# Kernel optimization log

Measured on AMD Instinct MI355X. Metric: run time of the kernel, lower is better.

The kernel has to match this reference:

```python
import jax, jax.numpy as jnp
import numpy as np

HEADS = 8
GS = 16
C = 512
E = 512
SCALE = (E / HEADS) ** -0.5
PNAMES = ['sa_qkv_w','sa_qkv_b','sa_pa_w','sa_pa_b','sa_ln1_g','sa_ln1_b','sa_f1_w','sa_f1_b','sa_f2_w','sa_f2_b','sa_ln2_g','sa_ln2_b','sa_c1_w','sa_c1_b','sa_c2_w','sa_c2_b','sa_bn_g','sa_bn_b','ca_q_w','ca_q_b','ca_k_w','ca_k_b','ca_v_w','ca_v_b','ca_pa_w','ca_pa_b','p_q_w','p_q_b','p_k_w','p_k_b','p_v_w','p_v_b','p_pa_w','p_pa_b','p_ln_g','p_ln_b','p_lin_w','p_lin_b']


def _ln(x, g, b, eps=1e-5):
    m = x.mean(-1, keepdims=True)
    v = jnp.var(x, axis=-1, keepdims=True)
    return (x - m) / jnp.sqrt(v + eps) * g + b


def _conv1x1(x, w, b):
    return jnp.einsum('bchw,oc->bohw', x, w) + b[None, :, None, None]


def _up_ac(x, out=GS):
    # bilinear upsample, align_corners=True (nn.UpsamplingBilinear2d)
    H = x.shape[2]
    pos = jnp.arange(out) * (H - 1) / (out - 1)
    lo = jnp.floor(pos).astype(jnp.int32)
    hi = jnp.minimum(lo + 1, H - 1)
    w = (pos - lo).astype(x.dtype)
    xr = x[:, :, lo, :] * (1 - w)[None, None, :, None] + x[:, :, hi, :] * w[None, None, :, None]
    return xr[:, :, :, lo] * (1 - w) + xr[:, :, :, hi] * w


def _asri(x, p):
    # Sequence_ASRI: GAP tokens -> attention over the batch axis -> pixel-shuffle back
    B = x.shape[0]; ch = E // HEADS
    gap = x.mean((2, 3))                                             # [B,C]
    qkv = (gap @ p['sa_qkv_w'].T + p['sa_qkv_b']).reshape(B, 4, ch, HEADS).transpose(1, 3, 0, 2)  # [4,H,B,ch]
    q, k, v, skip = qkv[0], qkv[1], qkv[2], qkv[3]
    attn = jax.nn.softmax(jnp.einsum('hbc,hdc->hbd', q, k) * SCALE, -1)  # [H,B,B]
    o = jnp.einsum('hbd,hdc->hbc', attn, v)
    merge = lambda t: t.transpose(1, 2, 0).reshape(B, E)             # 'head b c -> b (c head)'
    a = merge(o) @ p['sa_pa_w'].T + p['sa_pa_b'] + merge(skip)
    h = jax.nn.relu(_ln(a, p['sa_ln1_g'], p['sa_ln1_b']) @ p['sa_f1_w'].T + p['sa_f1_b'])
    a = h @ p['sa_f2_w'].T + p['sa_f2_b'] + a
    s = _ln(a, p['sa_ln2_g'], p['sa_ln2_b']) @ p['sa_c1_w'].T + p['sa_c1_b']  # [B,C*16]
    s = _up_ac(s.reshape(B, C, 4, 4))                                 # pixel shuffle p1=p2=4 then bilinear to 16x16
    s = _conv1x1(s, p['sa_c2_w'], p['sa_c2_b'])
    # BatchNorm2d in eval mode (running_mean=0, running_var=1, eps=1e-5)
    s = s / np.float32(np.sqrt(1.0 + 1e-5)) * p['sa_bn_g'][None, :, None, None] + p['sa_bn_b'][None, :, None, None]
    return x + jax.nn.relu(s)


def _sscm(x1, x2, p):
    # Sequence_SSCM: GAP-token q/k over batch axis, full spatial v
    B = x1.shape[0]; ch = E // HEADS
    q = (x1.mean((2, 3)) @ p['ca_q_w'].T + p['ca_q_b']).reshape(B, ch, HEADS).transpose(2, 0, 1)  # [H,B,ch]
    k = (x2.mean((2, 3)) @ p['ca_k_w'].T + p['ca_k_b']).reshape(B, ch, HEADS).transpose(2, 0, 1)
    v = _conv1x1(x2, p['ca_v_w'], p['ca_v_b']).reshape(B, ch, HEADS, GS, GS).transpose(2, 0, 1, 3, 4).reshape(HEADS, B, ch * GS * GS)
    attn = jax.nn.softmax(jnp.einsum('hbc,hdc->hbd', q, k) * SCALE, -1)  # [H,B,B]
    o = jnp.einsum('hbd,hdm->hbm', attn, v)
    o = o.reshape(HEADS, B, ch, GS, GS).transpose(1, 2, 0, 3, 4).reshape(B, E, GS, GS)
    return jax.nn.relu(_conv1x1(o, p['ca_pa_w'], p['ca_pa_b']))


def _pixel(x1, x2, p):
    # Pixel_SSCM: pixel-wise cross-batch attention (no scale -- matches source)
    B = x1.shape[0]; ch = E // HEADS; N = GS * GS
    split = lambda t: t.reshape(B, ch, HEADS, N).transpose(2, 0, 3, 1)   # 'b (c head) h w -> head b (h w) c'
    q = split(_conv1x1(x1, p['p_q_w'], p['p_q_b']))                      # [H,B,N,ch]
    k = split(_conv1x1(x2, p['p_k_w'], p['p_k_b']))
    v = split(_conv1x1(x2, p['p_v_w'], p['p_v_b'])).reshape(HEADS, B * N, ch)
    attn = jax.nn.softmax(jnp.einsum('hbnc,hqmc->hbqnm', q, k), -1)      # [H,B,B,N,N]
    attn = attn.transpose(1, 0, 3, 2, 4).reshape(B, HEADS, N, B * N)     # 'head b q h w -> b head h (q w)'
    o = jnp.einsum('bhnm,hmc->bhnc', attn, v)
    o = o.transpose(0, 3, 1, 2).reshape(B, E, GS, GS)                    # 'b head (h w) c -> b (c head) h w'
    o = _conv1x1(o, p['p_pa_w'], p['p_pa_b']) + x1
    t = o.reshape(B, C, N).transpose(0, 2, 1)                            # [B,N,C]
    t = jax.nn.relu(_ln(t, p['p_ln_g'], p['p_ln_b']) @ p['p_lin_w'].T + p['p_lin_b'])
    return t.transpose(0, 2, 1).reshape(B, C, GS, GS)


def _hrlm(p, xs, xq):
    sa_s = _asri(xs, p)
    sa_q = _asri(xq, p)
    ca_s = _sscm(sa_s, sa_q, p)
    ca_q = _sscm(sa_q, sa_s, p)
    return _pixel(sa_s, ca_q, p), _pixel(sa_q, ca_s, p)


def setup_inputs():
    key = jax.random.key(0)
    ks = iter(jax.random.split(key, 64))
    w = lambda *s: (jax.random.normal(next(ks), s) * 0.02).astype(jnp.float32)
    z = lambda n: jnp.zeros((n,), jnp.float32)
    o = lambda n: jnp.ones((n,), jnp.float32)
    return dict(
        fea_support=jax.random.normal(next(ks), (8, C, GS, GS), jnp.float32),
        fea_query=jax.random.normal(next(ks), (8, C, GS, GS), jnp.float32),
        sa_qkv_w=w(4 * E, C), sa_qkv_b=z(4 * E),
        sa_pa_w=w(E, E), sa_pa_b=z(E),
        sa_ln1_g=o(E), sa_ln1_b=z(E),
        sa_f1_w=w(E, E), sa_f1_b=z(E), sa_f2_w=w(E, E), sa_f2_b=z(E),
        sa_ln2_g=o(E), sa_ln2_b=z(E),
        sa_c1_w=w(C * 16, E), sa_c1_b=z(C * 16),
        sa_c2_w=w(C, E), sa_c2_b=z(C),
        sa_bn_g=o(C), sa_bn_b=z(C),
        ca_q_w=w(E, C), ca_q_b=z(E), ca_k_w=w(E, C), ca_k_b=z(E),
        ca_v_w=w(E, C), ca_v_b=z(E), ca_pa_w=w(C, E), ca_pa_b=z(C),
        p_q_w=w(E, C), p_q_b=z(E), p_k_w=w(E, C), p_k_b=z(E),
        p_v_w=w(E, C), p_v_b=z(E), p_pa_w=w(C, E), p_pa_b=z(C),
        p_ln_g=o(C), p_ln_b=z(C), p_lin_w=w(C, C), p_lin_b=z(C),
    )


def reference(fea_support, fea_query, sa_qkv_w, sa_qkv_b, sa_pa_w, sa_pa_b, sa_ln1_g, sa_ln1_b, sa_f1_w, sa_f1_b, sa_f2_w, sa_f2_b, sa_ln2_g, sa_ln2_b, sa_c1_w, sa_c1_b, sa_c2_w, sa_c2_b, sa_bn_g, sa_bn_b, ca_q_w, ca_q_b, ca_k_w, ca_k_b, ca_v_w, ca_v_b, ca_pa_w, ca_pa_b, p_q_w, p_q_b, p_k_w, p_k_b, p_v_w, p_v_b, p_pa_w, p_pa_b, p_ln_g, p_ln_b, p_lin_w, p_lin_b):
    p = dict(zip(PNAMES, (sa_qkv_w, sa_qkv_b, sa_pa_w, sa_pa_b, sa_ln1_g, sa_ln1_b, sa_f1_w, sa_f1_b, sa_f2_w, sa_f2_b, sa_ln2_g, sa_ln2_b, sa_c1_w, sa_c1_b, sa_c2_w, sa_c2_b, sa_bn_g, sa_bn_b, ca_q_w, ca_q_b, ca_k_w, ca_k_b, ca_v_w, ca_v_b, ca_pa_w, ca_pa_b, p_q_w, p_q_b, p_k_w, p_k_b, p_v_w, p_v_b, p_pa_w, p_pa_b, p_ln_g, p_ln_b, p_lin_w, p_lin_b)))
    return _hrlm(p, fea_support, fea_query)
```

## Files before the change

kernel.cpp:

```cpp
#include <hip/hip_runtime.h>
#include <cmath>

#define IMG 131072
#define BIGF 1048576

#define CF_RELU 1
#define CF_RES  2
#define CF_BN   4

typedef __attribute__((ext_vector_type(8))) short short8;
typedef __attribute__((ext_vector_type(4))) short short4v;
typedef __attribute__((ext_vector_type(4))) float f32x4;

__device__ __forceinline__ float wave_sum(float v){
    #pragma unroll
    for (int off = 32; off; off >>= 1) v += __shfl_xor(v, off);
    return v;
}

__device__ __forceinline__ unsigned short bf16_rn(float x){
    union { float f; unsigned u; } v; v.f = x;
    unsigned r = v.u + 0x7FFF + ((v.u >> 16) & 1);
    return (unsigned short)(r >> 16);
}
__device__ __forceinline__ float bf16_to_f(unsigned short h){
    union { float f; unsigned u; } v; v.u = ((unsigned)h) << 16;
    return v.f;
}

struct GapJobs  { const float* x[2]; float* o[2]; };
struct G8Job    { const float* in; const float* W; const float* bias; const float* add; float* out; };
struct G8Jobs   { G8Job j[4]; };
struct AAJobs   { const float* qkv[2]; float* om[2]; };
struct LnJobs   { const float* in[2]; float* out[2]; };
struct UpJobs   { const float* in[2]; float* out[2]; };
struct SAJobs   { const float* q8[2]; const float* k8[2]; float* aw[2]; };
struct SPJobs   { const float* aw[2]; const float* v[2]; float* out[2]; };
struct ZJobs    { float* p[2]; };
struct ConvJob  { const float* X; const float* W; const float* B; const float* R;
                  const float* bng; const float* bnb; float* O; int flags; };
struct ConvJobs { ConvJob j[6]; };
struct PixJob   { const float* Q; const float* K; const float* V; float* O; };
struct PixJobs  { PixJob j[2]; };

__global__ __launch_bounds__(64) void k_gap(GapJobs jo){
    const int br = blockIdx.y;
    const int bc = blockIdx.x;
    const int lane = threadIdx.x;
    const float* p = jo.x[br] + (size_t)bc * 256;
    float s = p[lane] + p[lane + 64] + p[lane + 128] + p[lane + 192];
    s = wave_sum(s);
    if (lane == 0) jo.o[br][bc] = s * (1.0f / 256.0f);
}

__global__ __launch_bounds__(64) void k_gemm8(G8Jobs jo, int add_off, int add_stride, int O, int relu){
    const G8Job j = jo.j[blockIdx.y];
    const int o = blockIdx.x;
    const int lane = threadIdx.x;
    const float* wr = j.W + (size_t)o * 512;
    float acc[8] = {0,0,0,0,0,0,0,0};
    #pragma unroll
    for (int i = 0; i < 8; i++){
        float w = wr[lane + 64*i];
        #pragma unroll
// ... 61 lines not shown
    }
}

__global__ __launch_bounds__(256) void k_up(UpJobs jo){
    const int br = blockIdx.y;
    const int idx = blockIdx.x*256 + threadIdx.x;
    const int x = idx & 15, y = (idx >> 4) & 15, bc = idx >> 8;
    float px = (float)(x*3) / 15.0f, py = (float)(y*3) / 15.0f;
    int lx = (int)px, ly = (int)py;
    float wx = px - lx, wy = py - ly;
    int hx = min(lx+1, 3), hy = min(ly+1, 3);
    const float* p = jo.in[br] + (size_t)bc * 16;
    float v00 = p[ly*4+lx], v01 = p[ly*4+hx], v10 = p[hy*4+lx], v11 = p[hy*4+hx];
    float a0 = v00*(1.f-wy) + v10*wy;
    float a1 = v01*(1.f-wy) + v11*wy;
    jo.out[br][idx] = a0*(1.f-wx) + a1*wx;
}

__global__ __launch_bounds__(256) void k_zero(ZJobs jo){
    jo.p[blockIdx.y][(size_t)blockIdx.x*256 + threadIdx.x] = 0.f;
}

#define LDK 40
__device__ __forceinline__ void convm_body(
    const float* __restrict__ Xb, const float* __restrict__ W,
    const float* __restrict__ bias, const float* __restrict__ resb,
    const float* __restrict__ bng, const float* __restrict__ bnb, float bninv,
    float* __restrict__ outb, int flags, int o0, int n0, unsigned short* lds)
{
    const int tid512 = threadIdx.x;
    const int g   = tid512 >> 8;
    const int tid = tid512 & 255;
    unsigned short* sAh = lds + g*10240;
    unsigned short* sAl = sAh + 2560;
    unsigned short* sBh = sAl + 2560;
    unsigned short* sBl = sBh + 2560;
    const int wv = tid >> 6, lane = tid & 63;
    const int quad = lane >> 4, l16 = lane & 15;
    const int wo = (wv >> 1) * 32, wn = (wv & 1) * 32;
    const int so  = tid >> 2, sk8 = (tid & 3) * 8;
    const int sp  = tid & 15, sn  = (tid >> 4) * 4;

    const float* wrow = W + (size_t)(o0 + so)*512 + g*256 + sk8;
    const float* xrow = Xb + (size_t)(g*256 + 2*sp)*256 + n0 + sn;

    f32x4 acc[2][2] = {};
    float4 a0 = *(const float4*)(wrow);
    float4 a1 = *(const float4*)(wrow + 4);
    float4 x0 = *(const float4*)(xrow);
    float4 x1 = *(const float4*)(xrow + 256);

    for (int k0 = 0; k0 < 256; k0 += 32){
        __syncthreads();
        {
            float wa[8] = {a0.x,a0.y,a0.z,a0.w,a1.x,a1.y,a1.z,a1.w};
            #pragma unroll
            for (int j = 0; j < 4; j++){
                unsigned short h0 = bf16_rn(wa[2*j]);
                unsigned short h1 = bf16_rn(wa[2*j+1]);
                unsigned short g0 = bf16_rn(wa[2*j]   - bf16_to_f(h0));
                unsigned short g1 = bf16_rn(wa[2*j+1] - bf16_to_f(h1));
                *(unsigned*)&sAh[so*LDK + sk8 + 2*j] = (unsigned)h0 | ((unsigned)h1 << 16);
                *(unsigned*)&sAl[so*LDK + sk8 + 2*j] = (unsigned)g0 | ((unsigned)g1 << 16);
            }
            float xe[4] = {x0.x,x0.y,x0.z,x0.w};
            float xo[4] = {x1.x,x1.y,x1.z,x1.w};
            #pragma unroll
            for (int j = 0; j < 4; j++){
                unsigned short h0 = bf16_rn(xe[j]);
                unsigned short h1 = bf16_rn(xo[j]);
                unsigned short g0 = bf16_rn(xe[j] - bf16_to_f(h0));
                unsigned short g1 = bf16_rn(xo[j] - bf16_to_f(h1));
                *(unsigned*)&sBh[(sn+j)*LDK + 2*sp] = (unsigned)h0 | ((unsigned)h1 << 16);
                *(unsigned*)&sBl[(sn+j)*LDK + 2*sp] = (unsigned)g0 | ((unsigned)g1 << 16);
            }
        }
        __syncthreads();
        if (k0 + 32 < 256){
            a0 = *(const float4*)(wrow + k0 + 32);
            a1 = *(const float4*)(wrow + k0 + 36);
            x0 = *(const float4*)(xrow + (size_t)(k0+32)*256);
            x1 = *(const float4*)(xrow + (size_t)(k0+32)*256 + 256);
        }
        short8 ah[2], al[2], bh[2], bl[2];
        #pragma unroll
        for (int t = 0; t < 2; t++){
            int ai = (wo + 16*t + l16)*LDK + quad*8;
            ah[t] = *(const short8*)&sAh[ai];
            al[t] = *(const short8*)&sAl[ai];
            int bi = (wn + 16*t + l16)*LDK + quad*8;
            bh[t] = *(const short8*)&sBh[bi];
            bl[t] = *(const short8*)&sBl[bi];
        }
        #pragma unroll
        for (int mt = 0; mt < 2; mt++){
            #pragma unroll
            for (int nt = 0; nt < 2; nt++){
// ... 7 lines not shown
    float* red = (float*)lds;
    if (g == 1){
        float* r = red + tid*20;
        #pragma unroll
        for (int mt = 0; mt < 2; mt++)
            #pragma unroll
            for (int nt = 0; nt < 2; nt++)
                *(f32x4*)(r + (mt*2+nt)*4) = acc[mt][nt];
    }
    __syncthreads();
    if (g == 0){
        float* r = red + tid*20;
        #pragma unroll
        for (int mt = 0; mt < 2; mt++)
            #pragma unroll
            for (int nt = 0; nt < 2; nt++){
                f32x4 o4 = *(const f32x4*)(r + (mt*2+nt)*4);
                acc[mt][nt] += o4;
            }
        #pragma unroll
        for (int mt = 0; mt < 2; mt++){
            #pragma unroll
            for (int nt = 0; nt < 2; nt++){
                const int n  = n0 + wn + 16*nt + l16;
                const int ob = o0 + wo + 16*mt + quad*4;
                #pragma unroll
                for (int rr = 0; rr < 4; rr++){
                    const int o = ob + rr;
                    float v = acc[mt][nt][rr] + bias[o];
                    if (flags & CF_BN)   v = v*(bninv*bng[o]) + bnb[o];
                    if (flags & CF_RELU) v = fmaxf(v, 0.f);
                    if (flags & CF_RES)  v += resb[(size_t)o*256 + n];
                    outb[(size_t)o*256 + n] = v;
                }
            }
        }
    }
}

__global__ __launch_bounds__(512) void k_convm(ConvJobs jo, float bninv)
{
    __shared__ unsigned short lds[20480];
    const int z = blockIdx.z;
    const ConvJob j = jo.j[z >> 3];
    const int b = z & 7;
    convm_body(j.X + (size_t)b*IMG, j.W, j.B, j.R ? j.R + (size_t)b*IMG : nullptr,
               j.bng, j.bnb, bninv, j.O + (size_t)b*IMG, j.flags,
               blockIdx.y*64, blockIdx.x*64, lds);
}

__global__ __launch_bounds__(64) void k_sscm_attn(SAJobs jo)
{
    const int br = blockIdx.y;
    const int h = blockIdx.x >> 3, b = blockIdx.x & 7, c = threadIdx.x;
    const int ci = c*8 + h;
    float qc = jo.q8[br][b*512 + ci];
    float s[8];
    #pragma unroll
    for (int d = 0; d < 8; d++){
        float p = qc * jo.k8[br][d*512 + ci];
        p = wave_sum(p);
        s[d] = p * 0.125f;
    }
// ... 7 lines not shown
    if (c < 8){
        float v = s[0];
        #pragma unroll
        for (int d = 1; d < 8; d++) if (c == d) v = s[d];
        jo.aw[br][blockIdx.x*8 + c] = v*r;
    }
}

__global__ __launch_bounds__(256) void k_sscm_apply(SPJobs jo)
{
    const int br = blockIdx.y;
    const int idx = blockIdx.x*256 + threadIdx.x;
    const int pix = idx & 255, e = (idx >> 8) & 511, b = idx >> 17;
    const int h = e & 7;
    const float* aw = jo.aw[br] + (h*8 + b)*8;
    const float* v = jo.v[br];
    float acc = 0.f;
    #pragma unroll
    for (int d = 0; d < 8; d++) acc += aw[d] * v[(size_t)d*IMG + (size_t)e*256 + pix];
    jo.out[br][idx] = acc;
}

__global__ __launch_bounds__(256) void k_pixel_mfma(PixJobs jo)
{
    __shared__ char smem[61440];
    unsigned short* sQh = (unsigned short*)smem;
    unsigned short* sQl = sQh + 2*64*40;
    unsigned short* sKh = sQl + 2*64*40;
    unsigned short* sKl = sKh + 2*128*40;
    unsigned short* sP  = (unsigned short*)smem;
    unsigned short* sVh = sP  + 4*64*40;
    unsigned short* sVl = sVh + 4*64*40;

    const int br = blockIdx.y >> 3, b = blockIdx.y & 7;
    const PixJob J = jo.j[br];
    const int nt = blockIdx.x & 3, d = blockIdx.x >> 2;
    const int h = blockIdx.z;
    const int tid = threadIdx.x;
    const int wv = tid >> 6, lane = tid & 63;
    const int quad = lane >> 4, l16 = lane & 15;
    const int n0 = nt * 64;
    const size_t bQ = (size_t)b * IMG;
    const size_t bK = (size_t)d * IMG;

    {
        const int q = tid & 63, c0 = tid >> 6;
        #pragma unroll
        for (int r = 0; r < 16; r++){
            int c = c0 + 4*r;
            float v = J.Q[bQ + (size_t)(c*8+h)*256 + n0 + q];
            unsigned short hi = bf16_rn(v);
            unsigned short lo = bf16_rn(v - bf16_to_f(hi));
            int idx = (c>>5)*2560 + q*40 + (c&31);
            sQh[idx] = hi; sQl[idx] = lo;
        }
    }
    {
        const int mloc = tid & 127, cb0 = tid >> 7;
        #pragma unroll
        for (int p = 0; p < 4; p++){
            int cb = cb0 + 2*p;
            short8 hi8, lo8;
            #pragma unroll
            for (int j = 0; j < 8; j++){
                float v = J.K[bK + (size_t)((cb*8+j)*8+h)*256 + mloc];
                unsigned short hv = bf16_rn(v);
                hi8[j] = (short)hv;
                lo8[j] = (short)bf16_rn(v - bf16_to_f(hv));
            }
            int idx = (cb>>2)*5120 + mloc*40 + (cb&3)*8;
            *(short8*)&sKh[idx] = hi8;
            *(short8*)&sKl[idx] = lo8;
        }
    }
    __syncthreads();

    short8 bqh[2], bql[2];
    #pragma unroll
    for (int ks = 0; ks < 2; ks++){
        int idx = ks*2560 + (wv*16 + l16)*40 + quad*8;
        bqh[ks] = *(const short8*)&sQh[idx];
        bql[ks] = *(const short8*)&sQl[idx];
    }

    f32x4 S[16] = {};
    #pragma unroll
    for (int hm = 0; hm < 2; hm++){
        if (hm == 1){
            __syncthreads();
            const int mloc = tid & 127, cb0 = tid >> 7;
            #pragma unroll
            for (int p = 0; p < 4; p++){
                int cb = cb0 + 2*p;
                short8 hi8, lo8;
                #pragma unroll
                for (int j = 0; j < 8; j++){
                    float v = J.K[bK + (size_t)((cb*8+j)*8+h)*256 + 128 + mloc];
                    unsigned short hv = bf16_rn(v);
                    hi8[j] = (short)hv;
                    lo8[j] = (short)bf16_rn(v - bf16_to_f(hv));
                }
                int idx = (cb>>2)*5120 + mloc*40 + (cb&3)*8;
                *(short8*)&sKh[idx] = hi8;
                *(short8*)&sKl[idx] = lo8;
            }
            __syncthreads();
        }
        #pragma unroll
        for (int mtl = 0; mtl < 8; mtl++){
            #pragma unroll
            for (int ks = 0; ks < 2; ks++){
                int idx = ks*5120 + (mtl*16 + l16)*40 + quad*8;
                short8 ah = *(const short8*)&sKh[idx];
                short8 al = *(const short8*)&sKl[idx];
                S[hm*8+mtl] = __builtin_amdgcn_mfma_f32_16x16x32_bf16(ah, bqh[ks], S[hm*8+mtl], 0, 0, 0);
// ... 30 lines not shown
    #pragma unroll
    for (int hm = 0; hm < 2; hm++){
        #pragma unroll
        for (int mtl = 0; mtl < 8; mtl++){
            short4v p4;
            #pragma unroll
            for (int r = 0; r < 4; r++) p4[r] = (short)bf16_rn(S[hm*8+mtl][r]);
            int idx = (mtl>>1)*2560 + (wv*16 + l16)*40 + 16*(mtl&1) + quad*4;
            *(short4v*)&sP[idx] = p4;
        }
        {
            const int mp = tid & 63, c0 = tid >> 6;
            #pragma unroll
            for (int p = 0; p < 16; p++){
                int c = c0 + 4*p;
                float2 vv = *(const float2*)&J.V[bK + (size_t)(c*8+h)*256 + hm*128 + 2*mp];
                unsigned short h0 = bf16_rn(vv.x), h1 = bf16_rn(vv.y);
                unsigned short g0 = bf16_rn(vv.x - bf16_to_f(h0));
                unsigned short g1 = bf16_rn(vv.y - bf16_to_f(h1));
                int idx = (mp>>4)*2560 + c*40 + ((2*mp)&31);
                *(unsigned*)&sVh[idx] = (unsigned)h0 | ((unsigned)h1 << 16);
                *(unsigned*)&sVl[idx] = (unsigned)g0 | ((unsigned)g1 << 16);
            }
        }
        __syncthreads();
        #pragma unroll
        for (int ks = 0; ks < 4; ks++){
            int pidx = ks*2560 + (wv*16 + l16)*40 + quad*8;
            short8 bp = *(const short8*)&sP[pidx];
            #pragma unroll
            for (int ct = 0; ct < 4; ct++){
                int vidx = ks*2560 + (ct*16 + l16)*40 + quad*8;
                short8 vh = *(const short8*)&sVh[vidx];
                short8 vl = *(const short8*)&sVl[vidx];
                oac[ct] = __builtin_amdgcn_mfma_f32_16x16x32_bf16(vh, bp, oac[ct], 0, 0, 0);
                oac[ct] = __builtin_amdgcn_mfma_f32_16x16x32_bf16(vl, bp, oac[ct], 0, 0, 0);
            }
        }
        __syncthreads();
    }

    const int q = n0 + wv*16 + l16;
    #pragma unroll
    for (int ct = 0; ct < 4; ct++){
        #pragma unroll
        for (int r = 0; r < 4; r++){
            int c = ct*16 + quad*4 + r;
            unsafeAtomicAdd(&J.O[bQ + (size_t)(c*8+h)*256 + q], oac[ct][r]);
        }
    }
}

__global__ __launch_bounds__(64) void k_ln_pix(LnJobs jo,
    const float* __restrict__ g, const float* __restrict__ be)
{
    const int br = blockIdx.y;
    const int bn = blockIdx.x;
    const int b = bn >> 8, n = bn & 255;
    const int lane = threadIdx.x;
    const float* p = jo.in[br] + (size_t)b*IMG + n;
    float v[8]; float s = 0.f;
    #pragma unroll
    for (int i = 0; i < 8; i++){ v[i] = p[(size_t)(lane + 64*i)*256]; s += v[i]; }
    s = wave_sum(s);
    float mean = s * (1.f/512.f);
    float q = 0.f;
    #pragma unroll
    for (int i = 0; i < 8; i++){ float d = v[i]-mean; q += d*d; }
    q = wave_sum(q);
    float rstd = rsqrtf(q*(1.f/512.f) + 1e-5f);
    #pragma unroll
    for (int i = 0; i < 8; i++){
        int c = lane + 64*i;
        jo.out[br][(size_t)b*IMG + (size_t)c*256 + n] = (v[i]-mean)*rstd*g[c] + be[c];
    }
}

extern "C" void kernel_launch(void* const* d_in, const int* in_sizes, int n_in,
                              void* d_out, int out_size, void* d_ws, size_t ws_size,
                              hipStream_t stream)
{
    const float* xs    = (const float*)d_in[0];
    const float* xq    = (const float*)d_in[1];
    const float* qkvw  = (const float*)d_in[2];  const float* qkvb = (const float*)d_in[3];
    const float* paw   = (const float*)d_in[4];  const float* pab  = (const float*)d_in[5];
    const float* ln1g  = (const float*)d_in[6];  const float* ln1b = (const float*)d_in[7];
    const float* f1w   = (const float*)d_in[8];  const float* f1b  = (const float*)d_in[9];
    const float* f2w   = (const float*)d_in[10]; const float* f2b  = (const float*)d_in[11];
    const float* ln2g  = (const float*)d_in[12]; const float* ln2b = (const float*)d_in[13];
    const float* c1w   = (const float*)d_in[14]; const float* c1b  = (const float*)d_in[15];
    const float* c2w   = (const float*)d_in[16]; const float* c2b  = (const float*)d_in[17];
    const float* bng   = (const float*)d_in[18]; const float* bnb  = (const float*)d_in[19];
    const float* caqw  = (const float*)d_in[20]; const float* caqb = (const float*)d_in[21];
    const float* cakw  = (const float*)d_in[22]; const float* cakb = (const float*)d_in[23];
    const float* cavw  = (const float*)d_in[24]; const float* cavb = (const float*)d_in[25];
    const float* capw  = (const float*)d_in[26]; const float* capb = (const float*)d_in[27];
    const float* pqw   = (const float*)d_in[28]; const float* pqb  = (const float*)d_in[29];
    const float* pkw   = (const float*)d_in[30]; const float* pkb  = (const float*)d_in[31];
    const float* pvw   = (const float*)d_in[32]; const float* pvb  = (const float*)d_in[33];
    const float* ppw   = (const float*)d_in[34]; const float* ppb  = (const float*)d_in[35];
    const float* plng  = (const float*)d_in[36]; const float* plnb = (const float*)d_in[37];
    const float* plinw = (const float*)d_in[38]; const float* plinb= (const float*)d_in[39];

    const size_t SMF = 262144;
    float* ws = (float*)d_ws;
    float* smb = ws;
    float* B[12];
    for (int i = 0; i < 12; i++) B[i] = ws + SMF + (size_t)i*BIGF;
    float* sa_s = B[0]; float* sa_q = B[1];
    float* ca_s = B[2]; float* ca_q = B[3];
    const bool paired_pixel = ws_size >= (SMF + 12*(size_t)BIGF)*sizeof(float) + 1024;

    auto SM = [&](int br){ return smb + (size_t)br*131072; };
    auto GAP=[&](int br){ return SM(br); };            auto QKV=[&](int br){ return SM(br)+4096; };
    auto OM =[&](int br){ return SM(br)+20480; };      auto AA =[&](int br){ return SM(br)+24576; };
    auto HB =[&](int br){ return SM(br)+28672; };      auto A2 =[&](int br){ return SM(br)+32768; };
    auto LNB=[&](int br){ return SM(br)+36864; };      auto S8 =[&](int br){ return SM(br)+40960; };
    auto ATW=[&](int br){ return SM(br)+106496; };     auto Q8 =[&](int br){ return SM(br)+107008; };
    auto K8 =[&](int br){ return SM(br)+111104; };

    const float bninv = 1.0f / sqrtf(1.0f + 1e-5f);
    float* out0 = (float*)d_out;
    float* out1 = out0 + (size_t)BIGF;

    {
        GapJobs gj = {{xs, xq}, {GAP(0), GAP(1)}};
        k_gap<<<dim3(4096,2), 64, 0, stream>>>(gj);
        G8Jobs qj = {{{GAP(0), qkvw, qkvb, nullptr, QKV(0)}, {GAP(1), qkvw, qkvb, nullptr, QKV(1)}}};
        k_gemm8<<<dim3(2048,2), 64, 0, stream>>>(qj, 0, 0, 2048, 0);
        AAJobs aj = {{QKV(0), QKV(1)}, {OM(0), OM(1)}};
        k_asri_attn<<<dim3(64,2), 64, 0, stream>>>(aj);
        G8Jobs pj = {{{OM(0), paw, pab, QKV(0), AA(0)}, {OM(1), paw, pab, QKV(1), AA(1)}}};
        k_gemm8<<<dim3(512,2), 64, 0, stream>>>(pj, 1536, 2048, 512, 0);
        LnJobs l1 = {{AA(0), AA(1)}, {LNB(0), LNB(1)}};
        k_ln8<<<dim3(8,2), 64, 0, stream>>>(l1, ln1g, ln1b);
        G8Jobs fj = {{{LNB(0), f1w, f1b, nullptr, HB(0)}, {LNB(1), f1w, f1b, nullptr, HB(1)}}};
        k_gemm8<<<dim3(512,2), 64, 0, stream>>>(fj, 0, 0, 512, 1);
        G8Jobs f2j = {{{HB(0), f2w, f2b, AA(0), A2(0)}, {HB(1), f2w, f2b, AA(1), A2(1)}}};
        k_gemm8<<<dim3(512,2), 64, 0, stream>>>(f2j, 0, 512, 512, 0);
        LnJobs l2 = {{A2(0), A2(1)}, {LNB(0), LNB(1)}};
        k_ln8<<<dim3(8,2), 64, 0, stream>>>(l2, ln2g, ln2b);
        G8Jobs cj = {{{LNB(0), c1w, c1b, nullptr, S8(0)}, {LNB(1), c1w, c1b, nullptr, S8(1)}}};
        k_gemm8<<<dim3(8192,2), 64, 0, stream>>>(cj, 0, 0, 8192, 0);
        UpJobs uj = {{S8(0), S8(1)}, {B[4], B[5]}};
        k_up<<<dim3(4096,2), 256, 0, stream>>>(uj);
        ConvJobs c2j = {};
        c2j.j[0] = {B[4], c2w, c2b, xs, bng, bnb, sa_s, CF_BN|CF_RELU|CF_RES};
        c2j.j[1] = {B[5], c2w, c2b, xq, bng, bnb, sa_q, CF_BN|CF_RELU|CF_RES};
        k_convm<<<dim3(4,8,16), 512, 0, stream>>>(c2j, bninv);
    }

    {
        GapJobs gj = {{sa_s, sa_q}, {GAP(0), GAP(1)}};
        k_gap<<<dim3(4096,2), 64, 0, stream>>>(gj);
        G8Jobs qj = {{{GAP(0), caqw, caqb, nullptr, Q8(0)},
                      {GAP(1), cakw, cakb, nullptr, K8(0)},
                      {GAP(1), caqw, caqb, nullptr, Q8(1)},
                      {GAP(0), cakw, cakb, nullptr, K8(1)}}};
        k_gemm8<<<dim3(512,4), 64, 0, stream>>>(qj, 0, 0, 512, 0);
        SAJobs sj = {{Q8(0), Q8(1)}, {K8(0), K8(1)}, {ATW(0), ATW(1)}};
        k_sscm_attn<<<dim3(64,2), 64, 0, stream>>>(sj);
        ConvJobs vj = {};
        vj.j[0] = {sa_q, cavw, cavb, nullptr, nullptr, nullptr, B[4], 0};
        vj.j[1] = {sa_s, cavw, cavb, nullptr, nullptr, nullptr, B[5], 0};
        k_convm<<<dim3(4,8,16), 512, 0, stream>>>(vj, 1.f);
        SPJobs pj = {{ATW(0), ATW(1)}, {B[4], B[5]}, {B[6], B[7]}};
        k_sscm_apply<<<dim3(4096,2), 256, 0, stream>>>(pj);
        ConvJobs aj = {};
        aj.j[0] = {B[6], capw, capb, nullptr, nullptr, nullptr, ca_s, CF_RELU};
        aj.j[1] = {B[7], capw, capb, nullptr, nullptr, nullptr, ca_q, CF_RELU};
        k_convm<<<dim3(4,8,16), 512, 0, stream>>>(aj, 1.f);
    }

    if (paired_pixel){
        ConvJobs qkvj = {};
        qkvj.j[0] = {sa_s, pqw, pqb, nullptr, nullptr, nullptr, B[4],  0};
        qkvj.j[1] = {ca_q, pkw, pkb, nullptr, nullptr, nullptr, B[5],  0};
        qkvj.j[2] = {ca_q, pvw, pvb, nullptr, nullptr, nullptr, B[6],  0};
        qkvj.j[3] = {sa_q, pqw, pqb, nullptr, nullptr, nullptr, B[8],  0};
        qkvj.j[4] = {ca_s, pkw, pkb, nullptr, nullptr, nullptr, B[9],  0};
        qkvj.j[5] = {ca_s, pvw, pvb, nullptr, nullptr, nullptr, B[10], 0};
        k_convm<<<dim3(4,8,48), 512, 0, stream>>>(qkvj, 1.f);
        ZJobs zj = {{B[7], B[11]}};
        k_zero<<<dim3(4096,2), 256, 0, stream>>>(zj);
        PixJobs pxj = {{{B[4], B[5], B[6], B[7]}, {B[8], B[9], B[10], B[11]}}};
        k_pixel_mfma<<<dim3(32,16,8), 256, 0, stream>>>(pxj);
        ConvJobs ppj = {};
        ppj.j[0] = {B[7],  ppw, ppb, sa_s, nullptr, nullptr, out0, CF_RES};
        ppj.j[1] = {B[11], ppw, ppb, sa_q, nullptr, nullptr, out1, CF_RES};
        k_convm<<<dim3(4,8,16), 512, 0, stream>>>(ppj, 1.f);
        LnJobs lj = {{out0, out1}, {B[4], B[8]}};
        k_ln_pix<<<dim3(2048,2), 64, 0, stream>>>(lj, plng, plnb);
        ConvJobs lnj = {};
        lnj.j[0] = {B[4], plinw, plinb, nullptr, nullptr, nullptr, out0, CF_RELU};
        lnj.j[1] = {B[8], plinw, plinb, nullptr, nullptr, nullptr, out1, CF_RELU};
        k_convm<<<dim3(4,8,16), 512, 0, stream>>>(lnj, 1.f);
    } else {
        auto pixel1 = [&](const float* x1, const float* x2, float* out){
            ConvJobs qkvj = {};
            qkvj.j[0] = {x1, pqw, pqb, nullptr, nullptr, nullptr, B[4], 0};
            qkvj.j[1] = {x2, pkw, pkb, nullptr, nullptr, nullptr, B[5], 0};
            qkvj.j[2] = {x2, pvw, pvb, nullptr, nullptr, nullptr, B[6], 0};
            k_convm<<<dim3(4,8,24), 512, 0, stream>>>(qkvj, 1.f);
            ZJobs zj = {{B[7], B[7]}};
            k_zero<<<dim3(4096,1), 256, 0, stream>>>(zj);
            PixJobs pxj = {{{B[4], B[5], B[6], B[7]}, {B[4], B[5], B[6], B[7]}}};
            k_pixel_mfma<<<dim3(32,8,8), 256, 0, stream>>>(pxj);
            ConvJobs ppj = {};
            ppj.j[0] = {B[7], ppw, ppb, x1, nullptr, nullptr, out, CF_RES};
            k_convm<<<dim3(4,8,8), 512, 0, stream>>>(ppj, 1.f);
            LnJobs lj = {{out, out}, {B[4], B[4]}};
            k_ln_pix<<<dim3(2048,1), 64, 0, stream>>>(lj, plng, plnb);
            ConvJobs lnj = {};
            lnj.j[0] = {B[4], plinw, plinb, nullptr, nullptr, nullptr, out, CF_RELU};
            k_convm<<<dim3(4,8,8), 512, 0, stream>>>(lnj, 1.f);
        };
        pixel1(sa_s, ca_q, out0);
        pixel1(sa_q, ca_s, out1);
    }

    (void)in_sizes; (void)n_in; (void)out_size;
}
```

Baseline: 480.7 us.

## Pre-split weights and activations into bf16 hi/lo pairs in producer epilogues

Weights are split once into bf16 hi/lo planes by a new kernel. Each producer kernel (upsample, conv epilogue, sscm_apply, layernorm, pixel attention output) now writes hi/lo bf16 planes directly, so the 1x1-conv GEMM and the pixel attention just copy pre-split data into LDS instead of converting fp32 in their inner loops. Intermediates move into a fixed global device pool, and the single-buffer fallback path is dropped. The cost is an extra split pass over the attention output and doubled writes for the split tensors. The weight split runs on every call.

```diff
diff --git a/kernel.cpp b/kernel.cpp
--- a/kernel.cpp
+++ b/kernel.cpp
@@ -3,13 +3,40 @@
 
 #define IMG 131072
 #define BIGF 1048576
-
-#define CF_RELU 1
-#define CF_RES  2
-#define CF_BN   4
+#define SBIG 1048576
+#define MB (1u<<20)
+#define TS (4u*MB)
+
+#define OFF_W   0u
+#define OFF_UP  (8u*MB)
+#define OFF_SAS (16u*MB)
+#define OFF_AP  (24u*MB)
+#define OFF_CA  (32u*MB)
+#define OFF_PQ  (40u*MB)
+#define OFF_PK  (48u*MB)
+#define OFF_PV  (56u*MB)
+#define OFF_OS  (64u*MB)
+#define OFF_LN  (72u*MB)
+#define OFF_FSA (80u*MB)
+#define OFF_FV  (88u*MB)
+#define OFF_FO  (96u*MB)
+
+__device__ __attribute__((aligned(256))) unsigned char g_pool[104u*MB];
+
+__device__ __forceinline__ unsigned short* SPL(size_t off){ return (unsigned short*)(g_pool + off); }
+__device__ __forceinline__ float* F32(size_t off){ return (float*)(g_pool + off); }
+
+#define CF_RELU  1
+#define CF_BN    2
+#define CF_RESE  4
+#define CF_RESP  8
+#define CF_OF32E 16
+#define CF_OF32P 32
+#define CF_OSPL  64
 
 typedef __attribute__((ext_vector_type(8))) short short8;
 typedef __attribute__((ext_vector_type(4))) short short4v;
+typedef __attribute__((ext_vector_type(4))) unsigned short ushort4v;
 typedef __attribute__((ext_vector_type(4))) float f32x4;
 
 __device__ __forceinline__ float wave_sum(float v){
@@ -17,7 +44,6 @@
     for (int off = 32; off; off >>= 1) v += __shfl_xor(v, off);
     return v;
 }
-
 __device__ __forceinline__ unsigned short bf16_rn(float x){
     union { float f; unsigned u; } v; v.f = x;
     unsigned r = v.u + 0x7FFF + ((v.u >> 16) & 1);
@@ -28,26 +54,66 @@
     return v.f;
 }
 
-struct GapJobs  { const float* x[2]; float* o[2]; };
+struct GapJobs  { const float* x[2]; size_t off[2]; float* o[2]; };
 struct G8Job    { const float* in; const float* W; const float* bias; const float* add; float* out; };
 struct G8Jobs   { G8Job j[4]; };
 struct AAJobs   { const float* qkv[2]; float* om[2]; };
 struct LnJobs   { const float* in[2]; float* out[2]; };
-struct UpJobs   { const float* in[2]; float* out[2]; };
+struct UpJobs   { const float* in[2]; };
 struct SAJobs   { const float* q8[2]; const float* k8[2]; float* aw[2]; };
-struct SPJobs   { const float* aw[2]; const float* v[2]; float* out[2]; };
-struct ZJobs    { float* p[2]; };
-struct ConvJob  { const float* X; const float* W; const float* B; const float* R;
-                  const float* bng; const float* bnb; float* O; int flags; };
+struct SPJobs   { const float* aw[2]; };
+struct W8       { const float* w[8]; };
+struct ConvJob  { size_t xoff, ooff, osoff, roff; const float* Rext; float* OextW;
+                  const float* Bp; int widx, flags; };
 struct ConvJobs { ConvJob j[6]; };
-struct PixJob   { const float* Q; const float* K; const float* V; float* O; };
-struct PixJobs  { PixJob j[2]; };
+struct PixLnJobs{ const float* in[2]; };
+
+__global__ __launch_bounds__(256) void k_splitw(W8 ws){
+    const int m = blockIdx.y;
+    const int i = (blockIdx.x*256 + threadIdx.x)*4;
+    float4 v = *(const float4*)(ws.w[m] + i);
+    unsigned short* WH = (unsigned short*)(g_pool + (size_t)m*1048576u);
+    unsigned short* WL = WH + 262144;
+    float vv[4] = {v.x, v.y, v.z, v.w};
+    ushort4v hi, lo;
+    #pragma unroll
+    for (int j = 0; j < 4; j++){
+        hi[j] = bf16_rn(vv[j]);
+        lo[j] = bf16_rn(vv[j] - bf16_to_f(hi[j]));
+    }
+    *(ushort4v*)&WH[i] = hi;
+    *(ushort4v*)&WL[i] = lo;
+}
+
+__global__ __launch_bounds__(256) void k_split_o(){
+    const int br = blockIdx.y;
+    const int i = (blockIdx.x*256 + threadIdx.x)*4;
+    const float* src = F32(OFF_FO + (size_t)br*TS);
+    unsigned short* H = SPL(OFF_OS + (size_t)br*TS);
+    float4 v = *(const float4*)(src + i);
+    float vv[4] = {v.x, v.y, v.z, v.w};
+    ushort4v hi, lo;
+    #pragma unroll
+    for (int j = 0; j < 4; j++){
+        hi[j] = bf16_rn(vv[j]);
+        lo[j] = bf16_rn(vv[j] - bf16_to_f(hi[j]));
+    }
+    *(ushort4v*)&H[i] = hi;
+    *(ushort4v*)&H[SBIG + i] = lo;
+}
+
+__global__ __launch_bounds__(256) void k_zero(){
+    float* p = F32(OFF_FO + (size_t)blockIdx.y*TS);
+    const int i = (blockIdx.x*256 + threadIdx.x)*4;
+    *(float4*)&p[i] = make_float4(0.f,0.f,0.f,0.f);
+}
 
 __global__ __launch_bounds__(64) void k_gap(GapJobs jo){
     const int br = blockIdx.y;
     const int bc = blockIdx.x;
     const int lane = threadIdx.x;
-    const float* p = jo.x[br] + (size_t)bc * 256;
+    const float* base = jo.x[br] ? jo.x[br] : F32(jo.off[br]);
+    const float* p = base + (size_t)bc * 256;
     float s = p[lane] + p[lane + 64] + p[lane + 128] + p[lane + 192];
     s = wave_sum(s);
     if (lane == 0) jo.o[br][bc] = s * (1.0f / 256.0f);
@@ -139,20 +205,23 @@
     float v00 = p[ly*4+lx], v01 = p[ly*4+hx], v10 = p[hy*4+lx], v11 = p[hy*4+hx];
     float a0 = v00*(1.f-wy) + v10*wy;
     float a1 = v01*(1.f-wy) + v11*wy;
-    jo.out[br][idx] = a0*(1.f-wx) + a1*wx;
-}
-
-__global__ __launch_bounds__(256) void k_zero(ZJobs jo){
-    jo.p[blockIdx.y][(size_t)blockIdx.x*256 + threadIdx.x] = 0.f;
+    float val = a0*(1.f-wx) + a1*wx;
+    unsigned short* H = SPL(OFF_UP + (size_t)br*TS);
+    unsigned short hi = bf16_rn(val);
+    H[idx] = hi;
+    H[SBIG + idx] = bf16_rn(val - bf16_to_f(hi));
 }
 
 #define LDK 40
-__device__ __forceinline__ void convm_body(
-    const float* __restrict__ Xb, const float* __restrict__ W,
-    const float* __restrict__ bias, const float* __restrict__ resb,
-    const float* __restrict__ bng, const float* __restrict__ bnb, float bninv,
-    float* __restrict__ outb, int flags, int o0, int n0, unsigned short* lds)
+__global__ __launch_bounds__(512) void k_convm(ConvJobs jo,
+    const float* __restrict__ bng, const float* __restrict__ bnb, float bninv)
 {
+    __shared__ unsigned short lds[20480];
+    const int z = blockIdx.z;
+    const ConvJob j = jo.j[z >> 3];
+    const int b = z & 7;
+    const int o0 = blockIdx.y*64, n0 = blockIdx.x*64;
+
     const int tid512 = threadIdx.x;
     const int g   = tid512 >> 8;
     const int tid = tid512 & 255;
@@ -166,46 +235,40 @@
     const int so  = tid >> 2, sk8 = (tid & 3) * 8;
     const int sp  = tid & 15, sn  = (tid >> 4) * 4;
 
-    const float* wrow = W + (size_t)(o0 + so)*512 + g*256 + sk8;
-    const float* xrow = Xb + (size_t)(g*256 + 2*sp)*256 + n0 + sn;
+    const unsigned short* WB = (const unsigned short*)(g_pool + (size_t)j.widx*1048576u);
+    const unsigned short* wrowH = WB + (size_t)(o0 + so)*512 + g*256 + sk8;
+    const unsigned short* wrowL = wrowH + 262144;
+    const unsigned short* XB = SPL(j.xoff) + (size_t)b*IMG;
+    const unsigned short* xrowH = XB + (size_t)(g*256 + 2*sp)*256 + n0 + sn;
+    const unsigned short* xrowL = xrowH + SBIG;
 
     f32x4 acc[2][2] = {};
-    float4 a0 = *(const float4*)(wrow);
-    float4 a1 = *(const float4*)(wrow + 4);
-    float4 x0 = *(const float4*)(xrow);
-    float4 x1 = *(const float4*)(xrow + 256);
+    short8   wh  = *(const short8*)wrowH;
+    short8   wl  = *(const short8*)wrowL;
+    ushort4v xh0 = *(const ushort4v*)(xrowH);
+    ushort4v xh1 = *(const ushort4v*)(xrowH + 256);
+    ushort4v xl0 = *(const ushort4v*)(xrowL);
+    ushort4v xl1 = *(const ushort4v*)(xrowL + 256);
 
     for (int k0 = 0; k0 < 256; k0 += 32){
         __syncthreads();
-        {
-            float wa[8] = {a0.x,a0.y,a0.z,a0.w,a1.x,a1.y,a1.z,a1.w};
-            #pragma unroll
-            for (int j = 0; j < 4; j++){
-                unsigned short h0 = bf16_rn(wa[2*j]);
-                unsigned short h1 = bf16_rn(wa[2*j+1]);
-                unsigned short g0 = bf16_rn(wa[2*j]   - bf16_to_f(h0));
-                unsigned short g1 = bf16_rn(wa[2*j+1] - bf16_to_f(h1));
-                *(unsigned*)&sAh[so*LDK + sk8 + 2*j] = (unsigned)h0 | ((unsigned)h1 << 16);
-                *(unsigned*)&sAl[so*LDK + sk8 + 2*j] = (unsigned)g0 | ((unsigned)g1 << 16);
-            }
-            float xe[4] = {x0.x,x0.y,x0.z,x0.w};
-            float xo[4] = {x1.x,x1.y,x1.z,x1.w};
-            #pragma unroll
-            for (int j = 0; j < 4; j++){
-                unsigned short h0 = bf16_rn(xe[j]);
-                unsigned short h1 = bf16_rn(xo[j]);
-                unsigned short g0 = bf16_rn(xe[j] - bf16_to_f(h0));
-                unsigned short g1 = bf16_rn(xo[j] - bf16_to_f(h1));
-                *(unsigned*)&sBh[(sn+j)*LDK + 2*sp] = (unsigned)h0 | ((unsigned)h1 << 16);
-                *(unsigned*)&sBl[(sn+j)*LDK + 2*sp] = (unsigned)g0 | ((unsigned)g1 << 16);
-            }
+        *(short8*)&sAh[so*LDK + sk8] = wh;
+        *(short8*)&sAl[so*LDK + sk8] = wl;
+        #pragma unroll
+        for (int t = 0; t < 4; t++){
+            *(unsigned*)&sBh[(sn+t)*LDK + 2*sp] =
+                (unsigned)(unsigned short)xh0[t] | ((unsigned)(unsigned short)xh1[t] << 16);
+            *(unsigned*)&sBl[(sn+t)*LDK + 2*sp] =
+                (unsigned)(unsigned short)xl0[t] | ((unsigned)(unsigned short)xl1[t] << 16);
         }
         __syncthreads();
         if (k0 + 32 < 256){
-            a0 = *(const float4*)(wrow + k0 + 32);
-            a1 = *(const float4*)(wrow + k0 + 36);
-            x0 = *(const float4*)(xrow + (size_t)(k0+32)*256);
-            x1 = *(const float4*)(xrow + (size_t)(k0+32)*256 + 256);
+            wh  = *(const short8*)(wrowH + k0 + 32);
+            wl  = *(const short8*)(wrowL + k0 + 32);
+            xh0 = *(const ushort4v*)(xrowH + (size_t)(k0+32)*256);
+            xh1 = *(const ushort4v*)(xrowH + (size_t)(k0+32)*256 + 256);
+            xl0 = *(const ushort4v*)(xrowL + (size_t)(k0+32)*256);
+            xl1 = *(const ushort4v*)(xrowL + (size_t)(k0+32)*256 + 256);
         }
         short8 ah[2], al[2], bh[2], bl[2];
         #pragma unroll
@@ -243,10 +306,18 @@
         #pragma unroll
         for (int mt = 0; mt < 2; mt++)
             #pragma unroll
-            for (int nt = 0; nt < 2; nt++){
-                f32x4 o4 = *(const f32x4*)(r + (mt*2+nt)*4);
-                acc[mt][nt] += o4;
-            }
+            for (int nt = 0; nt < 2; nt++)
+                acc[mt][nt] += *(const f32x4*)(r + (mt*2+nt)*4);
+
+        const int flags = j.flags;
+        const float* resb = nullptr;
+        if (flags & CF_RESE) resb = j.Rext + (size_t)b*IMG;
+        if (flags & CF_RESP) resb = F32(j.roff) + (size_t)b*IMG;
+        float* of32 = nullptr;
+        if (flags & CF_OF32E) of32 = j.OextW + (size_t)b*IMG;
+        if (flags & CF_OF32P) of32 = F32(j.ooff) + (size_t)b*IMG;
+        unsigned short* osH = (flags & CF_OSPL) ? SPL(j.osoff) + (size_t)b*IMG : nullptr;
+
         #pragma unroll
         for (int mt = 0; mt < 2; mt++){
             #pragma unroll
@@ -256,26 +327,21 @@
                 #pragma unroll
                 for (int rr = 0; rr < 4; rr++){
                     const int o = ob + rr;
-                    float v = acc[mt][nt][rr] + bias[o];
+                    float v = acc[mt][nt][rr] + j.Bp[o];
                     if (flags & CF_BN)   v = v*(bninv*bng[o]) + bnb[o];
                     if (flags & CF_RELU) v = fmaxf(v, 0.f);
-                    if (flags & CF_RES)  v += resb[(size_t)o*256 + n];
-                    outb[(size_t)o*256 + n] = v;
+                    if (resb) v += resb[(size_t)o*256 + n];
+                    const size_t oi = (size_t)o*256 + n;
+                    if (of32) of32[oi] = v;
+                    if (osH){
+                        unsigned short hi = bf16_rn(v);
+                        osH[oi] = hi;
+                        osH[SBIG + oi] = bf16_rn(v - bf16_to_f(hi));
+                    }
                 }
             }
         }
     }
-}
-
-__global__ __launch_bounds__(512) void k_convm(ConvJobs jo, float bninv)
-{
-    __shared__ unsigned short lds[20480];
-    const int z = blockIdx.z;
-    const ConvJob j = jo.j[z >> 3];
-    const int b = z & 7;
-    convm_body(j.X + (size_t)b*IMG, j.W, j.B, j.R ? j.R + (size_t)b*IMG : nullptr,
-               j.bng, j.bnb, bninv, j.O + (size_t)b*IMG, j.flags,
-               blockIdx.y*64, blockIdx.x*64, lds);
 }
 
 __global__ __launch_bounds__(64) void k_sscm_attn(SAJobs jo)
@@ -313,14 +379,17 @@
     const int pix = idx & 255, e = (idx >> 8) & 511, b = idx >> 17;
     const int h = e & 7;
     const float* aw = jo.aw[br] + (h*8 + b)*8;
-    const float* v = jo.v[br];
+    const float* v = F32(OFF_FV + (size_t)br*TS);
     float acc = 0.f;
     #pragma unroll
     for (int d = 0; d < 8; d++) acc += aw[d] * v[(size_t)d*IMG + (size_t)e*256 + pix];
-    jo.out[br][idx] = acc;
-}
-
-__global__ __launch_bounds__(256) void k_pixel_mfma(PixJobs jo)
+    unsigned short* H = SPL(OFF_AP + (size_t)br*TS);
+    unsigned short hi = bf16_rn(acc);
+    H[idx] = hi;
+    H[SBIG + idx] = bf16_rn(acc - bf16_to_f(hi));
+}
+
+__global__ __launch_bounds__(256) void k_pixel_mfma()
 {
     __shared__ char smem[61440];
     unsigned short* sQh = (unsigned short*)smem;
@@ -332,7 +401,11 @@
     unsigned short* sVl = sVh + 4*64*40;
 
     const int br = blockIdx.y >> 3, b = blockIdx.y & 7;
-    const PixJob J = jo.j[br];
+    const unsigned short* Qs = SPL(OFF_PQ + (size_t)br*TS);
+    const unsigned short* Ks = SPL(OFF_PK + (size_t)br*TS);
+    const unsigned short* Vs = SPL(OFF_PV + (size_t)br*TS);
+    float* O = F32(OFF_FO + (size_t)br*TS);
+
     const int nt = blockIdx.x & 3, d = blockIdx.x >> 2;
     const int h = blockIdx.z;
     const int tid = threadIdx.x;
@@ -347,11 +420,10 @@
         #pragma unroll
         for (int r = 0; r < 16; r++){
             int c = c0 + 4*r;
-            float v = J.Q[bQ + (size_t)(c*8+h)*256 + n0 + q];
-            unsigned short hi = bf16_rn(v);
-            unsigned short lo = bf16_rn(v - bf16_to_f(hi));
+            size_t gi = bQ + (size_t)(c*8+h)*256 + n0 + q;
             int idx = (c>>5)*2560 + q*40 + (c&31);
-            sQh[idx] = hi; sQl[idx] = lo;
+            sQh[idx] = Qs[gi];
+            sQl[idx] = Qs[SBIG + gi];
         }
     }
     {
@@ -362,10 +434,9 @@
             short8 hi8, lo8;
             #pragma unroll
             for (int j = 0; j < 8; j++){
-                float v = J.K[bK + (size_t)((cb*8+j)*8+h)*256 + mloc];
-                unsigned short hv = bf16_rn(v);
-                hi8[j] = (short)hv;
-                lo8[j] = (short)bf16_rn(v - bf16_to_f(hv));
+                size_t gi = bK + (size_t)((cb*8+j)*8+h)*256 + mloc;
+                hi8[j] = (short)Ks[gi];
+                lo8[j] = (short)Ks[SBIG + gi];
             }
             int idx = (cb>>2)*5120 + mloc*40 + (cb&3)*8;
             *(short8*)&sKh[idx] = hi8;
@@ -394,10 +465,9 @@
                 short8 hi8, lo8;
                 #pragma unroll
                 for (int j = 0; j < 8; j++){
-                    float v = J.K[bK + (size_t)((cb*8+j)*8+h)*256 + 128 + mloc];
-                    unsigned short hv = bf16_rn(v);
-                    hi8[j] = (short)hv;
-                    lo8[j] = (short)bf16_rn(v - bf16_to_f(hv));
+                    size_t gi = bK + (size_t)((cb*8+j)*8+h)*256 + 128 + mloc;
+                    hi8[j] = (short)Ks[gi];
+                    lo8[j] = (short)Ks[SBIG + gi];
                 }
                 int idx = (cb>>2)*5120 + mloc*40 + (cb&3)*8;
                 *(short8*)&sKh[idx] = hi8;
@@ -458,13 +528,10 @@
             #pragma unroll
             for (int p = 0; p < 16; p++){
                 int c = c0 + 4*p;
-                float2 vv = *(const float2*)&J.V[bK + (size_t)(c*8+h)*256 + hm*128 + 2*mp];
-                unsigned short h0 = bf16_rn(vv.x), h1 = bf16_rn(vv.y);
-                unsigned short g0 = bf16_rn(vv.x - bf16_to_f(h0));
-                unsigned short g1 = bf16_rn(vv.y - bf16_to_f(h1));
+                size_t gi = bK + (size_t)(c*8+h)*256 + hm*128 + 2*mp;
                 int idx = (mp>>4)*2560 + c*40 + ((2*mp)&31);
-                *(unsigned*)&sVh[idx] = (unsigned)h0 | ((unsigned)h1 << 16);
-                *(unsigned*)&sVl[idx] = (unsigned)g0 | ((unsigned)g1 << 16);
+                *(unsigned*)&sVh[idx] = *(const unsigned*)&Vs[gi];
+                *(unsigned*)&sVl[idx] = *(const unsigned*)&Vs[SBIG + gi];
             }
         }
         __syncthreads();
@@ -490,12 +557,12 @@
         #pragma unroll
         for (int r = 0; r < 4; r++){
             int c = ct*16 + quad*4 + r;
-            unsafeAtomicAdd(&J.O[bQ + (size_t)(c*8+h)*256 + q], oac[ct][r]);
-        }
-    }
-}
-
-__global__ __launch_bounds__(64) void k_ln_pix(LnJobs jo,
+            unsafeAtomicAdd(&O[bQ + (size_t)(c*8+h)*256 + q], oac[ct][r]);
+        }
+    }
+}
+
+__global__ __launch_bounds__(64) void k_ln_pix(PixLnJobs jo,
     const float* __restrict__ g, const float* __restrict__ be)
 {
     const int br = blockIdx.y;
@@ -503,6 +570,7 @@
     const int b = bn >> 8, n = bn & 255;
     const int lane = threadIdx.x;
     const float* p = jo.in[br] + (size_t)b*IMG + n;
+    unsigned short* H = SPL(OFF_LN + (size_t)br*TS);
     float v[8]; float s = 0.f;
     #pragma unroll
     for (int i = 0; i < 8; i++){ v[i] = p[(size_t)(lane + 64*i)*256]; s += v[i]; }
@@ -516,7 +584,11 @@
     #pragma unroll
     for (int i = 0; i < 8; i++){
         int c = lane + 64*i;
-        jo.out[br][(size_t)b*IMG + (size_t)c*256 + n] = (v[i]-mean)*rstd*g[c] + be[c];
+        float val = (v[i]-mean)*rstd*g[c] + be[c];
+        size_t oi = (size_t)b*IMG + (size_t)c*256 + n;
+        unsigned short hi = bf16_rn(val);
+        H[oi] = hi;
+        H[SBIG + oi] = bf16_rn(val - bf16_to_f(hi));
     }
 }
 
@@ -546,15 +618,7 @@
     const float* plng  = (const float*)d_in[36]; const float* plnb = (const float*)d_in[37];
     const float* plinw = (const float*)d_in[38]; const float* plinb= (const float*)d_in[39];
 
-    const size_t SMF = 262144;
-    float* ws = (float*)d_ws;
-    float* smb = ws;
-    float* B[12];
-    for (int i = 0; i < 12; i++) B[i] = ws + SMF + (size_t)i*BIGF;
-    float* sa_s = B[0]; float* sa_q = B[1];
-    float* ca_s = B[2]; float* ca_q = B[3];
-    const bool paired_pixel = ws_size >= (SMF + 12*(size_t)BIGF)*sizeof(float) + 1024;
-
+    float* smb = (float*)d_ws;
     auto SM = [&](int br){ return smb + (size_t)br*131072; };
     auto GAP=[&](int br){ return SM(br); };            auto QKV=[&](int br){ return SM(br)+4096; };
     auto OM =[&](int br){ return SM(br)+20480; };      auto AA =[&](int br){ return SM(br)+24576; };
@@ -567,8 +631,11 @@
     float* out0 = (float*)d_out;
     float* out1 = out0 + (size_t)BIGF;
 
+    W8 w8 = {{c2w, cavw, capw, pqw, pkw, pvw, ppw, plinw}};
+    k_splitw<<<dim3(256,8), 256, 0, stream>>>(w8);
+
     {
-        GapJobs gj = {{xs, xq}, {GAP(0), GAP(1)}};
+        GapJobs gj = {{xs, xq}, {0,0}, {GAP(0), GAP(1)}};
         k_gap<<<dim3(4096,2), 64, 0, stream>>>(gj);
         G8Jobs qj = {{{GAP(0), qkvw, qkvb, nullptr, QKV(0)}, {GAP(1), qkvw, qkvb, nullptr, QKV(1)}}};
         k_gemm8<<<dim3(2048,2), 64, 0, stream>>>(qj, 0, 0, 2048, 0);
@@ -586,16 +653,18 @@
         k_ln8<<<dim3(8,2), 64, 0, stream>>>(l2, ln2g, ln2b);
         G8Jobs cj = {{{LNB(0), c1w, c1b, nullptr, S8(0)}, {LNB(1), c1w, c1b, nullptr, S8(1)}}};
         k_gemm8<<<dim3(8192,2), 64, 0, stream>>>(cj, 0, 0, 8192, 0);
-        UpJobs uj = {{S8(0), S8(1)}, {B[4], B[5]}};
+        UpJobs uj = {{S8(0), S8(1)}};
         k_up<<<dim3(4096,2), 256, 0, stream>>>(uj);
         ConvJobs c2j = {};
-        c2j.j[0] = {B[4], c2w, c2b, xs, bng, bnb, sa_s, CF_BN|CF_RELU|CF_RES};
-        c2j.j[1] = {B[5], c2w, c2b, xq, bng, bnb, sa_q, CF_BN|CF_RELU|CF_RES};
-        k_convm<<<dim3(4,8,16), 512, 0, stream>>>(c2j, bninv);
+        c2j.j[0] = {OFF_UP + 0*TS, OFF_FSA + 0*TS, OFF_SAS + 0*TS, 0, xs, nullptr, c2b, 0,
+                    CF_BN|CF_RELU|CF_RESE|CF_OF32P|CF_OSPL};
+        c2j.j[1] = {OFF_UP + 1*TS, OFF_FSA + 1*TS, OFF_SAS + 1*TS, 0, xq, nullptr, c2b, 0,
+                    CF_BN|CF_RELU|CF_RESE|CF_OF32P|CF_OSPL};
+        k_convm<<<dim3(4,8,16), 512, 0, stream>>>(c2j, bng, bnb, bninv);
     }
 
     {
-        GapJobs gj = {{sa_s, sa_q}, {GAP(0), GAP(1)}};
+        GapJobs gj = {{nullptr, nullptr}, {OFF_FSA + 0*TS, OFF_FSA + 1*TS}, {GAP(0), GAP(1)}};
         k_gap<<<dim3(4096,2), 64, 0, stream>>>(gj);
         G8Jobs qj = {{{GAP(0), caqw, caqb, nullptr, Q8(0)},
                       {GAP(1), cakw, cakb, nullptr, K8(0)},
@@ -605,63 +674,40 @@
         SAJobs sj = {{Q8(0), Q8(1)}, {K8(0), K8(1)}, {ATW(0), ATW(1)}};
         k_sscm_attn<<<dim3(64,2), 64, 0, stream>>>(sj);
         ConvJobs vj = {};
-        vj.j[0] = {sa_q, cavw, cavb, nullptr, nullptr, nullptr, B[4], 0};
-        vj.j[1] = {sa_s, cavw, cavb, nullptr, nullptr, nullptr, B[5], 0};
-        k_convm<<<dim3(4,8,16), 512, 0, stream>>>(vj, 1.f);
-        SPJobs pj = {{ATW(0), ATW(1)}, {B[4], B[5]}, {B[6], B[7]}};
+        vj.j[0] = {OFF_SAS + 1*TS, OFF_FV + 0*TS, 0, 0, nullptr, nullptr, cavb, 1, CF_OF32P};
+        vj.j[1] = {OFF_SAS + 0*TS, OFF_FV + 1*TS, 0, 0, nullptr, nullptr, cavb, 1, CF_OF32P};
+        k_convm<<<dim3(4,8,16), 512, 0, stream>>>(vj, bng, bnb, 1.f);
+        SPJobs pj = {{ATW(0), ATW(1)}};
         k_sscm_apply<<<dim3(4096,2), 256, 0, stream>>>(pj);
         ConvJobs aj = {};
-        aj.j[0] = {B[6], capw, capb, nullptr, nullptr, nullptr, ca_s, CF_RELU};
-        aj.j[1] = {B[7], capw, capb, nullptr, nullptr, nullptr, ca_q, CF_RELU};
-        k_convm<<<dim3(4,8,16), 512, 0, stream>>>(aj, 1.f);
-    }
-
-    if (paired_pixel){
+        aj.j[0] = {OFF_AP + 0*TS, 0, OFF_CA + 0*TS, 0, nullptr, nullptr, capb, 2, CF_RELU|CF_OSPL};
+        aj.j[1] = {OFF_AP + 1*TS, 0, OFF_CA + 1*TS, 0, nullptr, nullptr, capb, 2, CF_RELU|CF_OSPL};
+        k_convm<<<dim3(4,8,16), 512, 0, stream>>>(aj, bng, bnb, 1.f);
+    }
+
+    {
         ConvJobs qkvj = {};
-        qkvj.j[0] = {sa_s, pqw, pqb, nullptr, nullptr, nullptr, B[4],  0};
-        qkvj.j[1] = {ca_q, pkw, pkb, nullptr, nullptr, nullptr, B[5],  0};
-        qkvj.j[2] = {ca_q, pvw, pvb, nullptr, nullptr, nullptr, B[6],  0};
-        qkvj.j[3] = {sa_q, pqw, pqb, nullptr, nullptr, nullptr, B[8],  0};
-        qkvj.j[4] = {ca_s, pkw, pkb, nullptr, nullptr, nullptr, B[9],  0};
-        qkvj.j[5] = {ca_s, pvw, pvb, nullptr, nullptr, nullptr, B[10], 0};
-        k_convm<<<dim3(4,8,48), 512, 0, stream>>>(qkvj, 1.f);
-        ZJobs zj = {{B[7], B[11]}};
-        k_zero<<<dim3(4096,2), 256, 0, stream>>>(zj);
-        PixJobs pxj = {{{B[4], B[5], B[6], B[7]}, {B[8], B[9], B[10], B[11]}}};
-        k_pixel_mfma<<<dim3(32,16,8), 256, 0, stream>>>(pxj);
+        qkvj.j[0] = {OFF_SAS + 0*TS, 0, OFF_PQ + 0*TS, 0, nullptr, nullptr, pqb, 3, CF_OSPL};
+        qkvj.j[1] = {OFF_CA  + 1*TS, 0, OFF_PK + 0*TS, 0, nullptr, nullptr, pkb, 4, CF_OSPL};
+        qkvj.j[2] = {OFF_CA  + 1*TS, 0, OFF_PV + 0*TS, 0, nullptr, nullptr, pvb, 5, CF_OSPL};
+        qkvj.j[3] = {OFF_SAS + 1*TS, 0, OFF_PQ + 1*TS, 0, nullptr, nullptr, pqb, 3, CF_OSPL};
+        qkvj.j[4] = {OFF_CA  + 0*TS, 0, OFF_PK + 1*TS, 0, nullptr, nullptr, pkb, 4, CF_OSPL};
+        qkvj.j[5] = {OFF_CA  + 0*TS, 0, OFF_PV + 1*TS, 0, nullptr, nullptr, pvb, 5, CF_OSPL};
+        k_convm<<<dim3(4,8,48), 512, 0, stream>>>(qkvj, bng, bnb, 1.f);
+        k_zero<<<dim3(1024,2), 256, 0, stream>>>();
+        k_pixel_mfma<<<dim3(32,16,8), 256, 0, stream>>>();
+        k_split_o<<<dim3(1024,2), 256, 0, stream>>>();
         ConvJobs ppj = {};
-        ppj.j[0] = {B[7],  ppw, ppb, sa_s, nullptr, nullptr, out0, CF_RES};
-        ppj.j[1] = {B[11], ppw, ppb, sa_q, nullptr, nullptr, out1, CF_RES};
-        k_convm<<<dim3(4,8,16), 512, 0, stream>>>(ppj, 1.f);
-        LnJobs lj = {{out0, out1}, {B[4], B[8]}};
+        ppj.j[0] = {OFF_OS + 0*TS, 0, 0, OFF_FSA + 0*TS, nullptr, out0, ppb, 6, CF_RESP|CF_OF32E};
+        ppj.j[1] = {OFF_OS + 1*TS, 0, 0, OFF_FSA + 1*TS, nullptr, out1, ppb, 6, CF_RESP|CF_OF32E};
+        k_convm<<<dim3(4,8,16), 512, 0, stream>>>(ppj, bng, bnb, 1.f);
+        PixLnJobs lj = {{out0, out1}};
         k_ln_pix<<<dim3(2048,2), 64, 0, stream>>>(lj, plng, plnb);
         ConvJobs lnj = {};
-        lnj.j[0] = {B[4], plinw, plinb, nullptr, nullptr, nullptr, out0, CF_RELU};
-        lnj.j[1] = {B[8], plinw, plinb, nullptr, nullptr, nullptr, out1, CF_RELU};
-        k_convm<<<dim3(4,8,16), 512, 0, stream>>>(lnj, 1.f);
-    } else {
-        auto pixel1 = [&](const float* x1, const float* x2, float* out){
-            ConvJobs qkvj = {};
-            qkvj.j[0] = {x1, pqw, pqb, nullptr, nullptr, nullptr, B[4], 0};
-            qkvj.j[1] = {x2, pkw, pkb, nullptr, nullptr, nullptr, B[5], 0};
-            qkvj.j[2] = {x2, pvw, pvb, nullptr, nullptr, nullptr, B[6], 0};
-            k_convm<<<dim3(4,8,24), 512, 0, stream>>>(qkvj, 1.f);
-            ZJobs zj = {{B[7], B[7]}};
-            k_zero<<<dim3(4096,1), 256, 0, stream>>>(zj);
-            PixJobs pxj = {{{B[4], B[5], B[6], B[7]}, {B[4], B[5], B[6], B[7]}}};
-            k_pixel_mfma<<<dim3(32,8,8), 256, 0, stream>>>(pxj);
-            ConvJobs ppj = {};
-            ppj.j[0] = {B[7], ppw, ppb, x1, nullptr, nullptr, out, CF_RES};
-            k_convm<<<dim3(4,8,8), 512, 0, stream>>>(ppj, 1.f);
-            LnJobs lj = {{out, out}, {B[4], B[4]}};
-            k_ln_pix<<<dim3(2048,1), 64, 0, stream>>>(lj, plng, plnb);
-            ConvJobs lnj = {};
-            lnj.j[0] = {B[4], plinw, plinb, nullptr, nullptr, nullptr, out, CF_RELU};
-            k_convm<<<dim3(4,8,8), 512, 0, stream>>>(lnj, 1.f);
-        };
-        pixel1(sa_s, ca_q, out0);
-        pixel1(sa_q, ca_s, out1);
-    }
-
-    (void)in_sizes; (void)n_in; (void)out_size;
-}
+        lnj.j[0] = {OFF_LN + 0*TS, 0, 0, 0, nullptr, out0, plinb, 7, CF_RELU|CF_OF32E};
+        lnj.j[1] = {OFF_LN + 1*TS, 0, 0, 0, nullptr, out1, plinb, 7, CF_RELU|CF_OF32E};
+        k_convm<<<dim3(4,8,16), 512, 0, stream>>>(lnj, bng, bnb, 1.f);
+    }
+
+    (void)in_sizes; (void)n_in; (void)out_size; (void)ws_size;
+}
```

Result: slower. 596.7 us (+24.1%).
